# Performance work log

Measured on AMD Instinct MI355X. Metric: run time of the kernel, lower is better.

Reference implementation:

```python
import jax, jax.numpy as jnp
import numpy as np

B = 256           # puzzles per batch
C = 128           # hidden_channels
L = 8             # num_layers
H, D = 4, 32      # heads, out per head (H*D == C, concat=True)
N_CELLS = 81
EPS_LN = 1e-5
NEG_SLOPE = 0.2   # PyG GATv2Conv default


def _sudoku_edges():
    # replicates GNNModel._create_sudoku_edges: row0=src, row1=dst, 1620 edges
    edges = []
    for r in range(9):
        for c in range(9):
            src = r * 9 + c
            nb = set()
            for k in range(9):
                if k != c:
                    nb.add(r * 9 + k)
                if k != r:
                    nb.add(k * 9 + c)
            br, bc = r // 3, c // 3
            for i in range(br * 3, br * 3 + 3):
                for j in range(bc * 3, bc * 3 + 3):
                    if i != r or j != c:
                        nb.add(i * 9 + j)
            for d in sorted(nb):
                edges.append((src, d))
    return np.array(edges, dtype=np.int32).T  # [2, 1620]


def setup_inputs() -> dict:
    key = jax.random.key(0)
    ks = jax.random.split(key, 8)
    base = _sudoku_edges()                                   # [2, 1620]
    shift = np.arange(B, dtype=np.int32) * N_CELLS
    ei = (base[:, None, :] + shift[None, :, None]).reshape(2, -1)  # [2, B*1620]
    s = 1.0 / np.sqrt(C)
    return {
        "x": jax.random.randint(ks[0], (B, 9, 9), 0, 10, dtype=jnp.int32),
        "edge_index": jnp.asarray(ei),
        "embed_w": jax.random.normal(ks[1], (10, C), jnp.float32) * 0.1,
        "Wl": jax.random.normal(ks[2], (L, C, C), jnp.float32) * s,
        "bl": jnp.zeros((L, C), jnp.float32),
        "Wr": jax.random.normal(ks[3], (L, C, C), jnp.float32) * s,
        "br": jnp.zeros((L, C), jnp.float32),
        "att": jax.random.normal(ks[4], (L, H, D), jnp.float32) * 0.1,
        "conv_b": jnp.zeros((L, C), jnp.float32),
        "ln_w": jnp.ones((L, C), jnp.float32),
        "ln_b": jnp.zeros((L, C), jnp.float32),
        "cls_w": jax.random.normal(ks[5], (C, 9), jnp.float32) * s,
        "cls_b": jnp.zeros((9,), jnp.float32),
    }


def _segment_softmax(logits, seg, n):
    # numerically stable per-destination-node softmax (PyG softmax semantics)
    m = jax.ops.segment_max(logits, seg, num_segments=n)
    e = jnp.exp(logits - m[seg])
    s = jax.ops.segment_sum(e, seg, num_segments=n)
    return e / (s[seg] + 1e-16)


def reference(x, edge_index, embed_w, Wl, bl, Wr, br, att, conv_b,
              ln_w, ln_b, cls_w, cls_b):
    N = B * N_CELLS
    h = embed_w[x.reshape(-1)]                               # [N, C]
    src, dst = edge_index[0], edge_index[1]
    for l in range(L):  # fixed small layer count
        h_in = h
        xl = (h @ Wl[l] + bl[l]).reshape(N, H, D)            # lin_l(x) -> values/src
        xr = (h @ Wr[l] + br[l]).reshape(N, H, D)            # lin_r(x) -> dst
        e = jax.nn.leaky_relu(xl[src] + xr[dst], NEG_SLOPE)  # [E, H, D]
        logits = jnp.einsum('ehd,hd->eh', e, att[l])         # [E, H]
        alpha = _segment_softmax(logits, dst, N)             # [E, H]
        out = jax.ops.segment_sum(xl[src] * alpha[..., None], dst,
                                  num_segments=N)            # [N, H, D]
        out = out.reshape(N, C) + conv_b[l]
        # PyG LayerNorm(mode='graph') with batch=None: global mean/std
        g = out - out.mean()
        g = g / (g.std() + EPS_LN)
        h = jax.nn.relu(g * ln_w[l] + ln_b[l]) + h_in        # dropout off (eval)
    logits = h @ cls_w + cls_b                               # [N, 9]
    return logits.reshape(B, 9, 9, 9)
```

## Files before the change

### kernel.cpp

```cpp
#include <hip/hip_runtime.h>
#include <string.h>

#define NPZ 81
#define NNODES 20736
#define CH 128
#define NHEAD 4
#define NB 20
#define NLAY 8
#define TPB 768

typedef __attribute__((ext_vector_type(4))) float f32x4;
typedef __attribute__((ext_vector_type(8))) __bf16 bf16x8;
typedef __attribute__((ext_vector_type(8))) unsigned short u16x8;

#define SW(n, hh, c4) ((c4) ^ (((n) & 7) ^ ((hh) << 1)))

__device__ __forceinline__ unsigned short f2bf(float f) {
  unsigned int u = __float_as_uint(f);
  u = (u + 0x7fffu + ((u >> 16) & 1u)) >> 16;
  return (unsigned short)u;
}

struct alignas(16) Slot { float s1, s2; unsigned int flag; unsigned int pad; };

__launch_bounds__(TPB, 3)
__global__ void k_fused(const int* __restrict__ x, const float* __restrict__ ew,
                        const float* __restrict__ Wl, const float* __restrict__ bl,
                        const float* __restrict__ Wr, const float* __restrict__ br,
                        const float* __restrict__ att, const float* __restrict__ convb,
                        const float* __restrict__ lnw, const float* __restrict__ lnb,
                        const float* __restrict__ clsw, const float* __restrict__ clsb,
                        u16x8* __restrict__ wpk, Slot* __restrict__ slots,
                        float* __restrict__ logits) {
  __shared__ float h_f[NPZ * 128];
  __shared__ unsigned short h_s[NPZ * 136];
  __shared__ float xl_s[NPZ * 128];
  __shared__ float xr_s[NPZ * 128];
  __shared__ int nb_s[NPZ * NB];
  __shared__ float att6_s[CH], att4_s[CH], cvb_s[CH], bias_s[256], lnw_s[CH], lnb_s[CH];
  __shared__ float al_s[NPZ * 4];
  __shared__ float red_s[26];

  const int tid = threadIdx.x;
  const int pz = blockIdx.x;
  const int n0 = pz * NPZ;

  if (tid < NPZ) {
    const int r = tid / 9, cq = tid % 9;
    int c2 = tid * NB;
    for (int k = 0; k < 9; ++k) if (k != cq) nb_s[c2++] = r * 9 + k;
    for (int k = 0; k < 9; ++k) if (k != r) nb_s[c2++] = k * 9 + cq;
    const int br0 = (r / 3) * 3, bc0 = (cq / 3) * 3;
    for (int i = br0; i < br0 + 3; ++i)
      for (int jj = bc0; jj < bc0 + 3; ++jj)
        if (i != r && jj != cq) nb_s[c2++] = i * 9 + jj;
  }

  for (int m = tid; m < NPZ * 32; m += TPB) {
    const int j = m >> 5, c4 = m & 31;
    const int xv = x[n0 + j];
    const f32x4 v = ((const f32x4*)ew)[xv * 32 + c4];
    *(f32x4*)&h_f[j * 128 + c4 * 4] = v;
    const unsigned int lo = (unsigned int)f2bf(v[0]) | ((unsigned int)f2bf(v[1]) << 16);
    const unsigned int hi = (unsigned int)f2bf(v[2]) | ((unsigned int)f2bf(v[3]) << 16);
    *(uint2*)&h_s[j * 136 + c4 * 4] = make_uint2(lo, hi);
  }

  if (tid < 128) {
    const int t = pz * 128 + tid;
    const int lane = t & 63;
    const int kb = (t >> 6) & 3;
    const int nt = (t >> 8) & 15;
    const int l = t >> 12;
    const int cc = nt * 16 + (lane & 15);
    const int k0 = kb * 32 + (lane >> 4) * 8;
    const float* W = (cc < CH) ? (Wl + (size_t)l * CH * CH + cc)
                               : (Wr + (size_t)l * CH * CH + (cc - CH));
    u16x8 v;
#pragma unroll
    for (int e = 0; e < 8; ++e) v[e] = f2bf(W[(size_t)(k0 + e) * CH]);
    unsigned long long w0, w1;
    memcpy(&w0, &v, 8);
    memcpy(&w1, ((const char*)&v) + 8, 8);
    unsigned long long* dst = (unsigned long long*)&wpk[t];
    __hip_atomic_store(&dst[0], w0, __ATOMIC_RELAXED, __HIP_MEMORY_SCOPE_AGENT);
    __hip_atomic_store(&dst[1], w1, __ATOMIC_RELAXED, __HIP_MEMORY_SCOPE_AGENT);
  }

  __syncthreads();
  if (tid == 0)
    __hip_atomic_store(&slots[8 * 256 + pz].flag, 1u, __ATOMIC_RELAXED, __HIP_MEMORY_SCOPE_AGENT);
  if (tid < 64) {
    bool done = false;
    while (!done) {
      bool ok = true;
#pragma unroll
      for (int q = 0; q < 4; ++q)
        ok &= (__hip_atomic_load(&slots[8 * 256 + tid + q * 64].flag, __ATOMIC_RELAXED,
                                 __HIP_MEMORY_SCOPE_AGENT) == 1u);
      done = __all(ok);
      if (!done) __builtin_amdgcn_s_sleep(1);
    }
  }
  __syncthreads();

  const int wv = tid >> 6, lane = tid & 63;
  const int l15 = lane & 15, l4 = lane >> 4;
  const int p = tid >> 1, half = tid & 1;
  const int j = p >> 2, hh = p & 3;
#define CQ(q) (hh * 32 + ((((q) << 1) | half) << 2))

#pragma unroll 1
  for (int l = 0; l < NLAY; ++l) {
    if (tid < 256) bias_s[tid] = (tid < CH) ? bl[l * CH + tid] : br[l * CH + tid - CH];
    else if (tid < 384) att6_s[tid - 256] = att[l * CH + (tid - 256)] * 0.6f;
    else if (tid < 512) att4_s[tid - 384] = att[l * CH + (tid - 384)] * 0.4f;
    else if (tid < 640) cvb_s[tid - 512] = convb[l * CH + (tid - 512)];
    else lnw_s[tid - 640] = lnw[l * CH + (tid - 640)];
    if (tid < 128) lnb_s[tid] = lnb[l * CH + tid];
    __syncthreads();

    {
      const int u0 = wv * 8;
      const int nt0 = u0 / 6;
      const int mt0 = u0 - nt0 * 6;
      const int split = 6 - mt0;
      bf16x8 b0[4], b1[4];
#pragma unroll
      for (int kb = 0; kb < 4; ++kb) {
        b0[kb] = ((const bf16x8*)wpk)[(((size_t)l * 16 + nt0) * 4 + kb) * 64 + lane];
        b1[kb] = ((const bf16x8*)wpk)[(((size_t)l * 16 + nt0 + 1) * 4 + kb) * 64 + lane];
      }
#pragma unroll 1
      for (int k = 0; k < split; ++k) {
        const int mt = mt0 + k;
        int arow = mt * 16 + l15; arow = arow > 80 ? 80 : arow;
        bf16x8 afr[4];
#pragma unroll
        for (int kb = 0; kb < 4; ++kb)
          afr[kb] = *(const bf16x8*)&h_s[arow * 136 + kb * 32 + l4 * 8];
        f32x4 acc = {0.f, 0.f, 0.f, 0.f};
#pragma unroll
        for (int kb = 0; kb < 4; ++kb)
          acc = __builtin_amdgcn_mfma_f32_16x16x32_bf16(afr[kb], b0[kb], acc, 0, 0, 0);
        const int cc = nt0 * 16 + l15;
        const float bia = bias_s[cc];
        float* dst = (cc < CH) ? xl_s : xr_s;
        const int c127 = cc & 127;
        const int dh = c127 >> 5;
        const int c4 = (c127 >> 2) & 7, el = c127 & 3;
#pragma unroll
        for (int i = 0; i < 4; ++i) {
          const int row = mt * 16 + l4 * 4 + i;
          if (row < NPZ)
            dst[row * 128 + dh * 32 + SW(row, dh, c4) * 4 + el] = acc[i] + bia;
        }
      }
#pragma unroll 1
      for (int k = 0; k < 8 - split; ++k) {
        const int mt = k;
        int arow = mt * 16 + l15; arow = arow > 80 ? 80 : arow;
        bf16x8 afr[4];
#pragma unroll
        for (int kb = 0; kb < 4; ++kb)
          afr[kb] = *(const bf16x8*)&h_s[arow * 136 + kb * 32 + l4 * 8];
        f32x4 acc = {0.f, 0.f, 0.f, 0.f};
#pragma unroll
        for (int kb = 0; kb < 4; ++kb)
          acc = __builtin_amdgcn_mfma_f32_16x16x32_bf16(afr[kb], b1[kb], acc, 0, 0, 0);
        const int cc = (nt0 + 1) * 16 + l15;
        const float bia = bias_s[cc];
        float* dst = (cc < CH) ? xl_s : xr_s;
        const int c127 = cc & 127;
        const int dh = c127 >> 5;
        const int c4 = (c127 >> 2) & 7, el = c127 & 3;
#pragma unroll
        for (int i = 0; i < 4; ++i) {
          const int row = mt * 16 + l4 * 4 + i;
          if (row < NPZ)
            dst[row * 128 + dh * 32 + SW(row, dh, c4) * 4 + el] = acc[i] + bia;
        }
      }
    }
    __syncthreads();

    f32x4 xr4[4], ar[4], o[4];
    float arj = 0.f;
    if (tid < NPZ * NHEAD * 2) {
      float alp = 0.f, arp = 0.f;
#pragma unroll
      for (int q = 0; q < 4; ++q) {
        const int c4 = (q << 1) | half;
        xr4[q] = *(const f32x4*)&xr_s[j * 128 + hh * 32 + SW(j, hh, c4) * 4];
        ar[q] = *(const f32x4*)&att4_s[CQ(q)];
        const f32x4 xv = *(const f32x4*)&xl_s[j * 128 + hh * 32 + SW(j, hh, c4) * 4];
        const f32x4 a6 = *(const f32x4*)&att6_s[CQ(q)];
#pragma unroll
        for (int e = 0; e < 4; ++e) {
          alp = fmaf(a6[e], xv[e], alp);
          arp = fmaf(a6[e], xr4[q][e], arp);
        }
      }
      alp += __shfl_xor(alp, 1, 64);
      arj = arp + __shfl_xor(arp, 1, 64);
      if (half == 0) al_s[j * 4 + hh] = alp;
    }
    __syncthreads();

    float psum = 0.f, psumsq = 0.f;
    if (tid < NPZ * NHEAD * 2) {
      float m = -3.0e38f, ssum = 0.f;
      f32x4 oacc[4] = {};
      for (int k = 0; k < NB; k += 2) {
        const int2 nbp = *(const int2*)&nb_s[j * NB + k];
        f32x4 v1[4], v2[4];
        float pa = 0.f, pb = 0.f;
#pragma unroll
        for (int q = 0; q < 4; ++q) {
          const int c4 = (q << 1) | half;
          v1[q] = *(const f32x4*)&xl_s[nbp.x * 128 + hh * 32 + SW(nbp.x, hh, c4) * 4];
          v2[q] = *(const f32x4*)&xl_s[nbp.y * 128 + hh * 32 + SW(nbp.y, hh, c4) * 4];
#pragma unroll
          for (int e = 0; e < 4; ++e) {
            pa = fmaf(ar[q][e], fabsf(v1[q][e] + xr4[q][e]), pa);
            pb = fmaf(ar[q][e], fabsf(v2[q][e] + xr4[q][e]), pb);
          }
        }
        const float lgA = al_s[nbp.x * 4 + hh] + arj + (pa + __shfl_xor(pa, 1, 64));
        const float lgB = al_s[nbp.y * 4 + hh] + arj + (pb + __shfl_xor(pb, 1, 64));
        const float nm = fmaxf(m, fmaxf(lgA, lgB));
        const float sc = __expf(m - nm);
        const float eA = __expf(lgA - nm);
        const float eB = __expf(lgB - nm);
        ssum = fmaf(ssum, sc, eA + eB);
#pragma unroll
        for (int q = 0; q < 4; ++q) {
          f32x4 t = oacc[q] * sc;
          t = v1[q] * eA + t;
          t = v2[q] * eB + t;
          oacc[q] = t;
        }
        m = nm;
      }
      const float rs = 1.f / ssum;
#pragma unroll
      for (int q = 0; q < 4; ++q) {
        o[q] = oacc[q] * rs + *(const f32x4*)&cvb_s[CQ(q)];
        psum += (o[q][0] + o[q][1]) + (o[q][2] + o[q][3]);
        psumsq += (o[q][0] * o[q][0] + o[q][1] * o[q][1]) +
                  (o[q][2] * o[q][2] + o[q][3] * o[q][3]);
      }
    }

#pragma unroll
    for (int mm = 1; mm < 64; mm <<= 1) {
      psum += __shfl_xor(psum, mm, 64);
      psumsq += __shfl_xor(psumsq, mm, 64);
    }
    if ((tid & 63) == 0) { red_s[wv * 2] = psum; red_s[wv * 2 + 1] = psumsq; }
    __syncthreads();

    if (tid >= 704) {
      const int pl = tid - 704;
      if (tid == 704) {
        float a = 0.f, b = 0.f;
#pragma unroll
        for (int i = 0; i < 12; ++i) { a += red_s[i * 2]; b += red_s[i * 2 + 1]; }
        Slot* sl = &slots[l * 256 + pz];
        const float2 f2 = make_float2(a, b);
        unsigned long long uv;
        memcpy(&uv, &f2, 8);
        __hip_atomic_store((unsigned long long*)&sl->s1, uv, __ATOMIC_RELAXED, __HIP_MEMORY_SCOPE_AGENT);
        asm volatile("s_waitcnt vmcnt(0)" ::: "memory");
        __hip_atomic_store(&sl->flag, 1u, __ATOMIC_RELAXED, __HIP_MEMORY_SCOPE_AGENT);
      }
      bool done = false;
      while (!done) {
        bool ok = true;
#pragma unroll
        for (int q = 0; q < 4; ++q)
          ok &= (__hip_atomic_load(&slots[l * 256 + pl + q * 64].flag, __ATOMIC_RELAXED,
                                   __HIP_MEMORY_SCOPE_AGENT) == 1u);
        done = __all(ok);
        if (!done) __builtin_amdgcn_s_sleep(1);
      }
      float s1 = 0.f, s2 = 0.f;
#pragma unroll
      for (int q = 0; q < 4; ++q) {
        const unsigned long long uv = __hip_atomic_load(
            (unsigned long long*)&slots[l * 256 + pl + q * 64].s1, __ATOMIC_RELAXED,
            __HIP_MEMORY_SCOPE_AGENT);
        float2 f2;
        memcpy(&f2, &uv, 8);
        s1 += f2.x; s2 += f2.y;
      }
#pragma unroll
      for (int mm = 1; mm < 64; mm <<= 1) {
        s1 += __shfl_xor(s1, mm, 64);
        s2 += __shfl_xor(s2, mm, 64);
      }
      if (tid == 704) {
        const float M = (float)NNODES * CH;
        const float mean = s1 / M;
        const float var = fmaxf(s2 / M - mean * mean, 0.f);
        red_s[24] = mean;
        red_s[25] = 1.f / (sqrtf(var) + 1e-5f);
      }
    }
    __syncthreads();
    const float mean = red_s[24], inv = red_s[25];

    if (tid < NPZ * NHEAD * 2) {
#pragma unroll
      for (int q = 0; q < 4; ++q) {
        const int cb = CQ(q);
        f32x4 hv = *(f32x4*)&h_f[j * 128 + cb];
#pragma unroll
        for (int e = 0; e < 4; ++e) {
          const float g = (o[q][e] - mean) * inv;
          hv[e] += fmaxf(g * lnw_s[cb + e] + lnb_s[cb + e], 0.f);
        }
        *(f32x4*)&h_f[j * 128 + cb] = hv;
        const unsigned int lo = (unsigned int)f2bf(hv[0]) | ((unsigned int)f2bf(hv[1]) << 16);
        const unsigned int hi = (unsigned int)f2bf(hv[2]) | ((unsigned int)f2bf(hv[3]) << 16);
        *(uint2*)&h_s[j * 136 + cb] = make_uint2(lo, hi);
      }
    }
    __syncthreads();
  }

  for (int idx = tid; idx < CH * 9; idx += TPB) {
    const int k = idx / 9, c = idx - k * 9;
    xr_s[k * 12 + c] = clsw[idx];
  }
  __syncthreads();
  for (int t2 = tid; t2 < NPZ * 9; t2 += TPB) {
    const int j2 = t2 / 9, c = t2 - j2 * 9;
    const int kc0 = tid & 31;
    float acc = clsb[c];
#pragma unroll 8
    for (int kc = 0; kc < 32; ++kc) {
      const int cc4 = (kc0 + kc) & 31;
      const f32x4 hv = *(const f32x4*)&h_f[j2 * 128 + cc4 * 4];
      acc += hv[0] * xr_s[(cc4 * 4 + 0) * 12 + c] + hv[1] * xr_s[(cc4 * 4 + 1) * 12 + c] +
             hv[2] * xr_s[(cc4 * 4 + 2) * 12 + c] + hv[3] * xr_s[(cc4 * 4 + 3) * 12 + c];
    }
    logits[(size_t)(n0 + j2) * 9 + c] = acc;
  }
}

extern "C" void kernel_launch(void* const* d_in, const int* in_sizes, int n_in,
                              void* d_out, int out_size, void* d_ws, size_t ws_size,
                              hipStream_t stream) {
  const int* x = (const int*)d_in[0];
  const float* ew = (const float*)d_in[2];
  const float* Wl = (const float*)d_in[3];
  const float* bl = (const float*)d_in[4];
  const float* Wr = (const float*)d_in[5];
  const float* br = (const float*)d_in[6];
  const float* att = (const float*)d_in[7];
  const float* cvb = (const float*)d_in[8];
  const float* lnw = (const float*)d_in[9];
  const float* lnb = (const float*)d_in[10];
  const float* clsw = (const float*)d_in[11];
  const float* clsb = (const float*)d_in[12];

  char* ws = (char*)d_ws;
  u16x8* wpk = (u16x8*)ws;
  Slot* slots = (Slot*)(ws + 524288);
  float* logits = (float*)d_out;

  (void)hipMemsetAsync(ws + 524288, 0, 9 * 256 * 16, stream);

  void* args[] = {(void*)&x, (void*)&ew, (void*)&Wl, (void*)&bl, (void*)&Wr, (void*)&br,
                  (void*)&att, (void*)&cvb, (void*)&lnw, (void*)&lnb, (void*)&clsw,
                  (void*)&clsb, (void*)&wpk, (void*)&slots, (void*)&logits};
  (void)hipLaunchCooperativeKernel((void*)k_fused, dim3(256), dim3(TPB), args, 0, stream);
}
```

Before: 172.0 us.

## Prefetch next-layer parameters during LayerNorm apply and regroup channel mapping

Per-layer parameters (biases, attention vectors, conv bias, LN weights) are now loaded for the next layer during the final LayerNorm/residual phase of the current layer. LN weights are double-buffered so the current layer's values stay intact. This removes one __syncthreads and exposed global-load latency at the start of each layer. Separately, the channel-to-thread mapping changes from interleaved float4 chunks to contiguous per-half chunks, which alters LDS access patterns and bank behaviour.

```diff
diff --git a/kernel.cpp b/kernel.cpp
--- a/kernel.cpp
+++ b/kernel.cpp
@@ -37,13 +37,21 @@
   __shared__ float xl_s[NPZ * 128];
   __shared__ float xr_s[NPZ * 128];
   __shared__ int nb_s[NPZ * NB];
-  __shared__ float att6_s[CH], att4_s[CH], cvb_s[CH], bias_s[256], lnw_s[CH], lnb_s[CH];
+  __shared__ float att6_s[CH], att4_s[CH], cvb_s[CH], bias_s[256];
+  __shared__ float lnw_s[2][CH], lnb_s[2][CH];
   __shared__ float al_s[NPZ * 4];
   __shared__ float red_s[26];
 
   const int tid = threadIdx.x;
   const int pz = blockIdx.x;
   const int n0 = pz * NPZ;
+
+  if (tid < 256) bias_s[tid] = (tid < CH) ? bl[tid] : br[tid - CH];
+  else if (tid < 384) att6_s[tid - 256] = att[tid - 256] * 0.6f;
+  else if (tid < 512) att4_s[tid - 384] = att[tid - 384] * 0.4f;
+  else if (tid < 640) cvb_s[tid - 512] = convb[tid - 512];
+  else lnw_s[0][tid - 640] = lnw[tid - 640];
+  if (tid < 128) lnb_s[0][tid] = lnb[tid];
 
   if (tid < NPZ) {
     const int r = tid / 9, cq = tid % 9;
@@ -108,18 +116,10 @@
   const int l15 = lane & 15, l4 = lane >> 4;
   const int p = tid >> 1, half = tid & 1;
   const int j = p >> 2, hh = p & 3;
-#define CQ(q) (hh * 32 + ((((q) << 1) | half) << 2))
+#define CQ(q) (hh * 32 + half * 16 + (q) * 4)
 
 #pragma unroll 1
   for (int l = 0; l < NLAY; ++l) {
-    if (tid < 256) bias_s[tid] = (tid < CH) ? bl[l * CH + tid] : br[l * CH + tid - CH];
-    else if (tid < 384) att6_s[tid - 256] = att[l * CH + (tid - 256)] * 0.6f;
-    else if (tid < 512) att4_s[tid - 384] = att[l * CH + (tid - 384)] * 0.4f;
-    else if (tid < 640) cvb_s[tid - 512] = convb[l * CH + (tid - 512)];
-    else lnw_s[tid - 640] = lnw[l * CH + (tid - 640)];
-    if (tid < 128) lnb_s[tid] = lnb[l * CH + tid];
-    __syncthreads();
-
     {
       const int u0 = wv * 8;
       const int nt0 = u0 / 6;
@@ -190,7 +190,7 @@
       float alp = 0.f, arp = 0.f;
 #pragma unroll
       for (int q = 0; q < 4; ++q) {
-        const int c4 = (q << 1) | half;
+        const int c4 = half * 4 + q;
         xr4[q] = *(const f32x4*)&xr_s[j * 128 + hh * 32 + SW(j, hh, c4) * 4];
         ar[q] = *(const f32x4*)&att4_s[CQ(q)];
         const f32x4 xv = *(const f32x4*)&xl_s[j * 128 + hh * 32 + SW(j, hh, c4) * 4];
@@ -217,7 +217,7 @@
         float pa = 0.f, pb = 0.f;
 #pragma unroll
         for (int q = 0; q < 4; ++q) {
-          const int c4 = (q << 1) | half;
+          const int c4 = half * 4 + q;
           v1[q] = *(const f32x4*)&xl_s[nbp.x * 128 + hh * 32 + SW(nbp.x, hh, c4) * 4];
           v2[q] = *(const f32x4*)&xl_s[nbp.y * 128 + hh * 32 + SW(nbp.y, hh, c4) * 4];
 #pragma unroll
@@ -310,7 +310,19 @@
     __syncthreads();
     const float mean = red_s[24], inv = red_s[25];
 
+    {
+      const int lp = (l < 7) ? l + 1 : 7;
+      const int pb = (l + 1) & 1;
+      if (tid < 256) bias_s[tid] = (tid < CH) ? bl[lp * CH + tid] : br[lp * CH + tid - CH];
+      else if (tid < 384) att6_s[tid - 256] = att[lp * CH + (tid - 256)] * 0.6f;
+      else if (tid < 512) att4_s[tid - 384] = att[lp * CH + (tid - 384)] * 0.4f;
+      else if (tid < 640) cvb_s[tid - 512] = convb[lp * CH + (tid - 512)];
+      else lnw_s[pb][tid - 640] = lnw[lp * CH + (tid - 640)];
+      if (tid < 128) lnb_s[pb][tid] = lnb[lp * CH + tid];
+    }
+
     if (tid < NPZ * NHEAD * 2) {
+      const int lb = l & 1;
 #pragma unroll
       for (int q = 0; q < 4; ++q) {
         const int cb = CQ(q);
@@ -318,7 +330,7 @@
 #pragma unroll
         for (int e = 0; e < 4; ++e) {
           const float g = (o[q][e] - mean) * inv;
-          hv[e] += fmaxf(g * lnw_s[cb + e] + lnb_s[cb + e], 0.f);
+          hv[e] += fmaxf(g * lnw_s[lb][cb + e] + lnb_s[lb][cb + e], 0.f);
         }
         *(f32x4*)&h_f[j * 128 + cb] = hv;
         const unsigned int lo = (unsigned int)f2bf(hv[0]) | ((unsigned int)f2bf(hv[1]) << 16);
```

After: 173.2 us. No clear change (+0.7%).
